# Performance work log

Measured on AMD Instinct MI355X. Metric: run time of the kernel, lower is better.

Reference implementation:

```python
import jax, jax.numpy as jnp
import numpy as np

B, T, DZ = 128, 512, 512  # batch, timesteps, latent state dim


def setup_inputs() -> dict:
    key = jax.random.key(0)
    k1, k2, k3 = jax.random.split(key, 3)
    t_inputs = jax.random.normal(k1, (B, T, 1), dtype=jnp.float32)      # per-step scalar time signal
    init_states = jax.random.normal(k2, (B, DZ), dtype=jnp.float32)     # initial latent state z_0
    f = jax.random.normal(k3, (1, DZ), dtype=jnp.float32) * 0.05        # learned weight f (D_in=1, D_z)
    return {"t_inputs": t_inputs, "init_states": init_states, "f": f}


def reference(t_inputs, init_states, f):
    # keras.backend.rnn with step: z_t = x_t * f + z_{t-1}
    # This linear recurrence is exactly a left-to-right prefix sum:
    #   z_t = z_0 + sum_{s<=t} x_s * f
    # outputs[1] of K.rnn is the full stacked sequence (B, T, DZ).
    increments = t_inputs * f                       # (B,T,1)*(1,DZ) -> (B,T,DZ)
    return init_states[:, None, :] + jnp.cumsum(increments, axis=1)
```

## Files before the change

### kernel.cpp

```cpp
#include <hip/hip_runtime.h>

#define BB 128
#define TT 512
#define DZ 512
#define ROWS_PER_BLOCK 32
#define NBLOCKS ((BB * TT) / ROWS_PER_BLOCK)

__global__ __launch_bounds__(256, 8) void lts_kernel(
    const float* __restrict__ t_in,
    const float* __restrict__ init,
    const float* __restrict__ f,
    float* __restrict__ out)
{
    __shared__ float s[TT];

    const int tid = threadIdx.x;
    const int g0  = blockIdx.x * ROWS_PER_BLOCK;
    const int b   = g0 >> 9;
    const int t0  = g0 & (TT - 1);

    if (tid < 64) {
        const float* xb = t_in + b * TT + tid * 8;
        const float4 a = *reinterpret_cast<const float4*>(xb);
        const float4 c = *reinterpret_cast<const float4*>(xb + 4);
        const float v0 = a.x;
        const float v1 = v0 + a.y;
        const float v2 = v1 + a.z;
        const float v3 = v2 + a.w;
        const float v4 = v3 + c.x;
        const float v5 = v4 + c.y;
        const float v6 = v5 + c.z;
        const float v7 = v6 + c.w;
        float run = v7;
#pragma unroll
        for (int off = 1; off < 64; off <<= 1) {
            const float y = __shfl_up(run, off, 64);
            if (tid >= off) run += y;
        }
        const float excl = run - v7;
        float4 o0, o1;
        o0.x = v0 + excl; o0.y = v1 + excl; o0.z = v2 + excl; o0.w = v3 + excl;
        o1.x = v4 + excl; o1.y = v5 + excl; o1.z = v6 + excl; o1.w = v7 + excl;
        *reinterpret_cast<float4*>(&s[tid * 8])     = o0;
        *reinterpret_cast<float4*>(&s[tid * 8 + 4]) = o1;
    }

    const int q = tid & 127;
    const int h = tid >> 7;
    const int d = q * 4;

    const float4 f4 = *reinterpret_cast<const float4*>(&f[d]);
    const float4 i4 = *reinterpret_cast<const float4*>(&init[b * DZ + d]);

    __syncthreads();

    float* outp = out + ((size_t)(g0 + h) * DZ + d);
#pragma unroll
    for (int iter = 0; iter < ROWS_PER_BLOCK / 2; ++iter) {
        const float st = s[t0 + iter * 2 + h];
        float4 o;
        o.x = i4.x + f4.x * st;
        o.y = i4.y + f4.y * st;
        o.z = i4.z + f4.z * st;
        o.w = i4.w + f4.w * st;
        *reinterpret_cast<float4*>(outp) = o;
        outp += 2 * DZ;
    }
}

extern "C" void kernel_launch(void* const* d_in, const int* in_sizes, int n_in,
                              void* d_out, int out_size, void* d_ws, size_t ws_size,
                              hipStream_t stream) {
    const float* t_in = (const float*)d_in[0];
    const float* init = (const float*)d_in[1];
    const float* f    = (const float*)d_in[2];
    float* out        = (float*)d_out;

    lts_kernel<<<dim3(NBLOCKS), dim3(256), 0, stream>>>(t_in, init, f, out);
}
```

Baseline: 26.31 us.

## Compute prefix scan in every wavefront and broadcast via readlane, drop LDS and barrier

Every wavefront now computes the full 512-step prefix sum of its batch row in registers, instead of only the first wave writing it to shared memory. Each output row's scalar is fetched with readlane from the owning lane, which removes the LDS buffer and the block-wide barrier. Output stores become nontemporal to avoid polluting cache with the write-only result. The cost is redundant scan work and input loads in all four waves.

```diff
diff --git a/kernel.cpp b/kernel.cpp
--- a/kernel.cpp
+++ b/kernel.cpp
@@ -3,8 +3,29 @@
 #define BB 128
 #define TT 512
 #define DZ 512
-#define ROWS_PER_BLOCK 32
-#define NBLOCKS ((BB * TT) / ROWS_PER_BLOCK)
+#define RPB 32
+#define NBLOCKS ((BB * TT) / RPB)
+
+typedef float f4_t __attribute__((ext_vector_type(4)));
+
+template<int H>
+__device__ __forceinline__ void store_rows(const float v[8], int lbase,
+                                           const f4_t f4, const f4_t i4,
+                                           float* outp) {
+#pragma unroll
+    for (int iter = 0; iter < RPB / 2; ++iter) {
+        const int toff = 2 * iter + H;
+        const float st = __int_as_float(__builtin_amdgcn_readlane(
+            __float_as_int(v[toff & 7]), lbase + (toff >> 3)));
+        f4_t o;
+        o.x = i4.x + f4.x * st;
+        o.y = i4.y + f4.y * st;
+        o.z = i4.z + f4.z * st;
+        o.w = i4.w + f4.w * st;
+        __builtin_nontemporal_store(o, reinterpret_cast<f4_t*>(outp));
+        outp += 2 * DZ;
+    }
+}
 
 __global__ __launch_bounds__(256, 8) void lts_kernel(
     const float* __restrict__ t_in,
@@ -12,60 +33,42 @@
     const float* __restrict__ f,
     float* __restrict__ out)
 {
-    __shared__ float s[TT];
+    const int tid  = threadIdx.x;
+    const int lane = tid & 63;
+    const int g0   = blockIdx.x * RPB;
+    const int b    = g0 >> 9;
+    const int t0   = g0 & (TT - 1);
 
-    const int tid = threadIdx.x;
-    const int g0  = blockIdx.x * ROWS_PER_BLOCK;
-    const int b   = g0 >> 9;
-    const int t0  = g0 & (TT - 1);
-
-    if (tid < 64) {
-        const float* xb = t_in + b * TT + tid * 8;
-        const float4 a = *reinterpret_cast<const float4*>(xb);
-        const float4 c = *reinterpret_cast<const float4*>(xb + 4);
-        const float v0 = a.x;
-        const float v1 = v0 + a.y;
-        const float v2 = v1 + a.z;
-        const float v3 = v2 + a.w;
-        const float v4 = v3 + c.x;
-        const float v5 = v4 + c.y;
-        const float v6 = v5 + c.z;
-        const float v7 = v6 + c.w;
-        float run = v7;
+    const float* xb = t_in + b * TT + lane * 8;
+    const f4_t a = *reinterpret_cast<const f4_t*>(xb);
+    const f4_t c = *reinterpret_cast<const f4_t*>(xb + 4);
+    float v[8];
+    v[0] = a.x;        v[1] = v[0] + a.y;
+    v[2] = v[1] + a.z; v[3] = v[2] + a.w;
+    v[4] = v[3] + c.x; v[5] = v[4] + c.y;
+    v[6] = v[5] + c.z; v[7] = v[6] + c.w;
+    float run = v[7];
 #pragma unroll
-        for (int off = 1; off < 64; off <<= 1) {
-            const float y = __shfl_up(run, off, 64);
-            if (tid >= off) run += y;
-        }
-        const float excl = run - v7;
-        float4 o0, o1;
-        o0.x = v0 + excl; o0.y = v1 + excl; o0.z = v2 + excl; o0.w = v3 + excl;
-        o1.x = v4 + excl; o1.y = v5 + excl; o1.z = v6 + excl; o1.w = v7 + excl;
-        *reinterpret_cast<float4*>(&s[tid * 8])     = o0;
-        *reinterpret_cast<float4*>(&s[tid * 8 + 4]) = o1;
+    for (int off = 1; off < 64; off <<= 1) {
+        const float y = __shfl_up(run, off, 64);
+        if (lane >= off) run += y;
     }
+    const float excl = run - v[7];
+#pragma unroll
+    for (int k = 0; k < 8; ++k) v[k] += excl;
 
     const int q = tid & 127;
     const int h = tid >> 7;
     const int d = q * 4;
 
-    const float4 f4 = *reinterpret_cast<const float4*>(&f[d]);
-    const float4 i4 = *reinterpret_cast<const float4*>(&init[b * DZ + d]);
-
-    __syncthreads();
+    const f4_t f4 = *reinterpret_cast<const f4_t*>(&f[d]);
+    const f4_t i4 = *reinterpret_cast<const f4_t*>(&init[b * DZ + d]);
 
     float* outp = out + ((size_t)(g0 + h) * DZ + d);
-#pragma unroll
-    for (int iter = 0; iter < ROWS_PER_BLOCK / 2; ++iter) {
-        const float st = s[t0 + iter * 2 + h];
-        float4 o;
-        o.x = i4.x + f4.x * st;
-        o.y = i4.y + f4.y * st;
-        o.z = i4.z + f4.z * st;
-        o.w = i4.w + f4.w * st;
-        *reinterpret_cast<float4*>(outp) = o;
-        outp += 2 * DZ;
-    }
+    const int lbase = t0 >> 3;
+
+    if (h == 0) store_rows<0>(v, lbase, f4, i4, outp);
+    else        store_rows<1>(v, lbase, f4, i4, outp);
 }
 
 extern "C" void kernel_launch(void* const* d_in, const int* in_sizes, int n_in,
```

Measured after the change: 29.94 us. 1.14x slower.
